# Kernel optimization log

Measured on AMD Instinct MI355X. Metric: run time of the kernel, lower is better.

## Reference

```python
import jax, jax.numpy as jnp
import numpy as np

MAX_REL = 30
N_HEADS = 8


def conv1d(x, w, b=None, groups=1):
    # x: [B, L, Cin], w: [Cout, Cin/groups, K]  (torch Conv1d layout), 'same' padding
    pad = w.shape[-1] // 2
    y = jax.lax.conv_general_dilated(
        x, w, window_strides=(1,), padding=[(pad, pad)],
        dimension_numbers=("NLC", "OIL", "NLC"), feature_group_count=groups)
    return y if b is None else y + b


def setup_inputs() -> dict:
    key = jax.random.key(0)
    ks = jax.random.split(key, 16)
    B, L, S = 8, 1024, 512          # L = 2 * S (required by Gamma.repeat(1,2,1))
    sd, vd, dm = 512, 64, 512       # spatial_dim == d_model (residual add)
    D = 3 * vd                      # rel-pos / K,V channel dim

    def n(k, shape, s):
        return (jax.random.normal(k, shape, jnp.float32) * s).astype(jnp.float32)

    return {
        "x_spatial": jax.random.normal(ks[0], (B, L, sd), jnp.float32),
        "x_velocity": jax.random.normal(ks[1], (B, S, vd), jnp.float32),
        "w_gamma": n(ks[2], (dm, vd, 1), 0.05)[:, :, 0],      # conv_gamma 1x1, no bias -> [dm, vd]
        "w3": n(ks[3], (vd, vd, 3), 0.07), "b3": jnp.zeros((vd,), jnp.float32),
        "w5": n(ks[4], (vd, vd, 5), 0.05), "b5": jnp.zeros((vd,), jnp.float32),
        "w7": n(ks[5], (vd, vd, 7), 0.04), "b7": jnp.zeros((vd,), jnp.float32),
        "rel_table": n(ks[6], (2 * MAX_REL + 1, D), 0.05),    # embedding [61, 192]
        "dw_w": n(ks[7], (D, 1, 3), 0.3), "dw_b": jnp.zeros((D,), jnp.float32),
        "wq": n(ks[8], (dm, sd), 0.03),
        "wk": n(ks[9], (dm, D), 0.05),
        "wv": n(ks[10], (dm, D), 0.05),
        "fc_w": n(ks[11], (dm, dm), 0.03), "fc_b": jnp.zeros((dm,), jnp.float32),
        "ln_g": jnp.ones((dm,), jnp.float32), "ln_b": jnp.zeros((dm,), jnp.float32),
    }


def rel_pos_enc(ms, rel_table, dw_w, dw_b):
    # Math-equivalent reduction of the torch O(B*S^2*D) op:
    # output[b,j] = mean_i where(i==j, dwconv_row_i(fused)[j], fused[b,i,j])
    #            = ms[b,j] + mean_i rel[i,j] + (diag_conv[b,j] - fused[b,j,j]) / S
    B, S, D = ms.shape
    pos = jnp.arange(S)
    idx = jnp.clip(pos[None, :] - pos[:, None], -MAX_REL, MAX_REL) + MAX_REL  # [S,S]
    mean_rel = rel_table[idx].mean(axis=0)                                    # [S,D]
    # fused[b,i,j] = ms[b,j] + rel_table[idx[i,j]]; diagonal uses idx = MAX_REL,
    # its +/-1 neighbors along j use MAX_REL -/+ ... -> rel[i,i-1]=MAX_REL-1, rel[i,i+1]=MAX_REL+1
    center = ms + rel_table[MAX_REL]                                          # fused[b,i,i]
    left = jnp.pad(ms[:, :-1] + rel_table[MAX_REL - 1], ((0, 0), (1, 0), (0, 0)))   # conv zero-pads at i=0
    right = jnp.pad(ms[:, 1:] + rel_table[MAX_REL + 1], ((0, 0), (0, 1), (0, 0)))   # conv zero-pads at i=S-1
    diag_conv = dw_w[:, 0, 0] * left + dw_w[:, 0, 1] * center + dw_w[:, 0, 2] * right + dw_b
    return ms + mean_rel[None] + (diag_conv - center) / S


def reference(x_spatial, x_velocity, w_gamma, w3, b3, w5, b5, w7, b7,
              rel_table, dw_w, dw_b, wq, wk, wv, fc_w, fc_b, ln_g, ln_b):
    B, S, vd = x_velocity.shape
    _, L, _ = x_spatial.shape
    dm = wq.shape[0]
    dk = dm // N_HEADS

    gamma = jax.nn.sigmoid(jnp.einsum("bsc,dc->bsd", x_velocity, w_gamma))   # [B,S,dm]

    ms = jnp.concatenate([conv1d(x_velocity, w3, b3),
                          conv1d(x_velocity, w5, b5),
                          conv1d(x_velocity, w7, b7)], axis=-1)              # [B,S,3vd]
    x_pe = rel_pos_enc(ms, rel_table, dw_w, dw_b)                            # [B,S,3vd]

    q = jnp.einsum("blc,dc->bld", x_spatial, wq).reshape(B, L, N_HEADS, dk).transpose(0, 2, 1, 3)
    k = jnp.einsum("bsc,dc->bsd", x_pe, wk).reshape(B, S, N_HEADS, dk).transpose(0, 2, 1, 3)
    v = jnp.einsum("bsc,dc->bsd", x_pe, wv).reshape(B, S, N_HEADS, dk).transpose(0, 2, 1, 3)

    scores = jnp.einsum("bhld,bhsd->bhls", q, k) / jnp.sqrt(jnp.float32(dk))
    attn = jax.nn.softmax(scores, axis=-1)                                   # dropout: eval mode (identity)
    out = jnp.einsum("bhls,bhsd->bhld", attn, v)                             # [B,H,L,dk]
    out = out.transpose(0, 2, 1, 3).reshape(B, L, dm)
    out = out @ fc_w.T + fc_b

    out = jnp.tile(gamma, (1, 2, 1)) * out                                   # L == 2*S
    res = x_spatial + out
    mu = res.mean(-1, keepdims=True)
    var = res.var(-1, keepdims=True)
    return (res - mu) / jnp.sqrt(var + 1e-5) * ln_g + ln_b
```

## Files before the change

kernel.cpp:

```cpp
#include <hip/hip_runtime.h>
#include <hip/hip_bf16.h>

constexpr int B  = 8;
constexpr int L  = 1024;
constexpr int S  = 512;
constexpr int VD = 64;
constexpr int DM = 512;
constexpr int D3 = 192;
constexpr int H  = 8;
constexpr int DK = 64;

typedef __attribute__((ext_vector_type(8))) short s8v;
typedef __attribute__((ext_vector_type(4))) float f4v;

__device__ inline unsigned short f2b(float f) {
    unsigned int u = __builtin_bit_cast(unsigned int, f);
    u += 0x7fffu + ((u >> 16) & 1u);
    return (unsigned short)(u >> 16);
}
__device__ inline float b2f(unsigned int lo16) {
    return __builtin_bit_cast(float, lo16 << 16);
}

__device__ __forceinline__ void gload16(const void* g, void* l) {
    __builtin_amdgcn_global_load_lds(
        (const __attribute__((address_space(1))) void*)g,
        (__attribute__((address_space(3))) void*)l, 16, 0, 0);
}

struct CastArgs {
    const float* src[7];
    unsigned short* dst[7];
    int n[7];
    float scale[7];
};

__global__ __launch_bounds__(256) void prep_cast_k(
    CastArgs a,
    const float* __restrict__ w3, const float* __restrict__ w5,
    const float* __restrict__ w7, const float* __restrict__ dw_w,
    const float* __restrict__ rel_table, const float* __restrict__ b3,
    const float* __restrict__ b5, const float* __restrict__ b7,
    const float* __restrict__ dw_b,
    unsigned short* __restrict__ WpeT, unsigned short* __restrict__ Cp)
{
    int t = threadIdx.x;
    int y = blockIdx.y;

    if (y < 7) {
        const float* s = a.src[y];
        unsigned short* d = a.dst[y];
        int n = a.n[y];
        float sc = a.scale[y];
        for (long i = (long)(blockIdx.x * 256 + t) * 4; i < n;
             i += (long)gridDim.x * 1024) {
            float4 f = *(const float4*)(s + i);
            ushort4 o;
            o.x = f2b(f.x * sc); o.y = f2b(f.y * sc);
            o.z = f2b(f.z * sc); o.w = f2b(f.w * sc);
            *(ushort4*)(d + i) = o;
        }
        return;
    }

    if (t >= 192) return;
    int o = t;
    float inv = 1.0f / S;

    if (blockIdx.x < 640) {
        int n = blockIdx.x;
        if (n >= 576) { WpeT[n * D3 + o] = 0; return; }
        int j = n >> 6, c = n & 63, delta = j - 4;
        const float* w; int KW, P, oo;
        if (o < 64)       { w = w3; KW = 3; P = 1; oo = o; }
        else if (o < 128) { w = w5; KW = 5; P = 2; oo = o - 64; }
        else              { w = w7; KW = 7; P = 3; oo = o - 128; }
        float mu0 = dw_w[o * 3 + 0] * inv;
        float mu1 = 1.f + (dw_w[o * 3 + 1] - 1.f) * inv;
        float mu2 = dw_w[o * 3 + 2] * inv;
        float acc = 0.f;
        int k;
        k = delta + 1 + P; if (k >= 0 && k < KW) acc += mu0 * w[(oo * 64 + c) * KW + k];
        k = delta + P;     if (k >= 0 && k < KW) acc += mu1 * w[(oo * 64 + c) * KW + k];
        k = delta - 1 + P; if (k >= 0 && k < KW) acc += mu2 * w[(oo * 64 + c) * KW + k];
        WpeT[n * D3 + o] = f2b(acc);
        return;
    }

    int j = blockIdx.x - 640;
    float acc = 0.f;
#pragma unroll
    for (int r = 1; r < 60; r++) {
        int i = j - (r - 30);
        if (i >= 0 && i < S) acc += rel_table[r * D3 + o];
    }
    float c60 = (float)max(0, j - 29);
    float c0  = (float)max(0, (S - 30) - j);
    acc += c60 * rel_table[60 * D3 + o] + c0 * rel_table[0 * D3 + o];
    float mean_rel = acc * inv;

    float bo  = (o < 64) ? b3[o] : (o < 128) ? b5[o - 64] : b7[o - 128];
    float dw0 = dw_w[o * 3], dw1 = dw_w[o * 3 + 1], dw2 = dw_w[o * 3 + 2];
    float r29 = rel_table[29 * D3 + o], r30 = rel_table[30 * D3 + o],
          r31 = rel_table[31 * D3 + o];
    float alpha = 1.f + (dw1 - 1.f) * inv, beta = dw0 * inv, gamma = dw2 * inv;

    float cp = mean_rel + bo * alpha + (dw1 * r30 + dw_b[o] - r30) * inv;
    if (j > 0)     cp += beta * bo + dw0 * r29 * inv;
    if (j < S - 1) cp += gamma * bo + dw2 * r31 * inv;
    Cp[j * D3 + o] = f2b(cp);
}

__global__ __launch_bounds__(256) void pre_gemm5_k(
    const unsigned short* __restrict__ wk_bf,
    const unsigned short* __restrict__ wv_bf,
    const unsigned short* __restrict__ WpeT,
    const unsigned short* __restrict__ Cp,
    const unsigned short* __restrict__ xv_bf,
    const unsigned short* __restrict__ wg_bf,
    unsigned short* __restrict__ WEff,
    unsigned short* __restrict__ Cb,
    unsigned short* __restrict__ gamma_bf)
{
    int z = blockIdx.z, mx = blockIdx.x, ny = blockIdx.y;
    const unsigned short *A, *Bm;
    unsigned short* C;
    int K, lda, ldb, ldc;
    if (z < 2) {
        if (mx >= 4) return;
        A = z ? wv_bf : wk_bf; Bm = WpeT; C = WEff + (long)z * DM * 640;
        K = D3; lda = D3; ldb = D3; ldc = 640;
    } else if (z < 4) {
        if (mx >= 4 || ny >= 4) return;
        A = Cp; Bm = (z == 2) ? wk_bf : wv_bf; C = Cb + (long)(z - 2) * S * DM;
        K = D3; lda = D3; ldb = D3; ldc = DM;
    } else {
        if (ny >= 4) return;
        A = xv_bf; Bm = wg_bf; C = gamma_bf;
        K = VD; lda = VD; ldb = VD; ldc = DM;
    }

    __shared__ __align__(16) unsigned short As[128 * 64];
    __shared__ __align__(16) unsigned short Bs[128 * 64];

    int t = threadIdx.x;
    int l = t & 63, w = t >> 6;
    int lx = l & 15, lh = l >> 4;
    int wr = w >> 1, wc = w & 1;
    int m0 = mx * 128, n0 = ny * 128;

    f4v acc[4][4] = {};

    for (int k0 = 0; k0 < K; k0 += 64) {
        __syncthreads();
#pragma unroll
        for (int p = 0; p < 4; p++) {
            int flat = p * 256 + t;
            int r = flat >> 3, c = flat & 7;
            int csw = (c ^ (r & 7)) * 8;
            gload16(A  + (long)(m0 + r) * lda + k0 + csw, As + flat * 8);
            gload16(Bm + (long)(n0 + r) * ldb + k0 + csw, Bs + flat * 8);
        }
        __syncthreads();
#pragma unroll
        for (int ks = 0; ks < 2; ks++) {
            s8v af[4], bf[4];
#pragma unroll
            for (int i = 0; i < 4; i++) {
                int ra = wr * 64 + i * 16 + lx;
                af[i] = *(const s8v*)(As + ra * 64 + (((ks * 4 + lh) ^ (ra & 7)) * 8));
                int rb = wc * 64 + i * 16 + lx;
                bf[i] = *(const s8v*)(Bs + rb * 64 + (((ks * 4 + lh) ^ (rb & 7)) * 8));
            }
#pragma unroll
            for (int i = 0; i < 4; i++)
#pragma unroll
                for (int j = 0; j < 4; j++)
                    acc[i][j] = __builtin_amdgcn_mfma_f32_16x16x32_bf16(
                        af[i], bf[j], acc[i][j], 0, 0, 0);
        }
    }

#pragma unroll
    for (int i = 0; i < 4; i++) {
#pragma unroll
        for (int r = 0; r < 4; r++) {
            int m = m0 + wr * 64 + i * 16 + lh * 4 + r;
#pragma unroll
            for (int j = 0; j < 4; j++) {
                int n = n0 + wc * 64 + j * 16 + lx;
                C[(long)m * ldc + n] = f2b(acc[i][j][r]);
            }
        }
    }
}

__global__ __launch_bounds__(256) void qconv_k(
    const unsigned short* __restrict__ xs_bf,
    const unsigned short* __restrict__ wq_bf,
    unsigned short* __restrict__ qbuf,
    const unsigned short* __restrict__ xvb,
    const unsigned short* __restrict__ Weff0,
    const unsigned short* __restrict__ bias0,
    unsigned short* __restrict__ Cout0,
    const unsigned short* __restrict__ zsrc)
{
    __shared__ __align__(16) unsigned short As[128 * 64];
    __shared__ __align__(16) unsigned short Bs[128 * 64];

    int zt = blockIdx.z;
    int t = threadIdx.x;
    int l = t & 63, w = t >> 6;
    int lx = l & 15, lh = l >> 4;
    int wr = w >> 1, wc = w & 1;

    f4v acc[4][4] = {};

    if (zt == 0) {
        int m0 = blockIdx.x * 128, n0 = blockIdx.y * 128;
        for (int k0 = 0; k0 < DM; k0 += 64) {
            __syncthreads();
#pragma unroll
            for (int p = 0; p < 4; p++) {
                int flat = p * 256 + t;
                int r = flat >> 3, c = flat & 7;
                int csw = (c ^ (r & 7)) * 8;
                gload16(xs_bf + (long)(m0 + r) * DM + k0 + csw, As + flat * 8);
                gload16(wq_bf + (long)(n0 + r) * DM + k0 + csw, Bs + flat * 8);
            }
            __syncthreads();
#pragma unroll
            for (int ks = 0; ks < 2; ks++) {
                s8v af[4], bf[4];
#pragma unroll
                for (int i = 0; i < 4; i++) {
                    int ra = wr * 64 + i * 16 + lx;
                    af[i] = *(const s8v*)(As + ra * 64 + (((ks * 4 + lh) ^ (ra & 7)) * 8));
                    int rb = wc * 64 + i * 16 + lx;
                    bf[i] = *(const s8v*)(Bs + rb * 64 + (((ks * 4 + lh) ^ (rb & 7)) * 8));
                }
#pragma unroll
                for (int i = 0; i < 4; i++)
#pragma unroll
                    for (int j = 0; j < 4; j++)
                        acc[i][j] = __builtin_amdgcn_mfma_f32_16x16x32_bf16(
                            af[i], bf[j], acc[i][j], 0, 0, 0);
            }
        }
#pragma unroll
        for (int i = 0; i < 4; i++) {
#pragma unroll
            for (int r = 0; r < 4; r++) {
                int m = m0 + wr * 64 + i * 16 + lh * 4 + r;
#pragma unroll
                for (int j = 0; j < 4; j++) {
                    int n = n0 + wc * 64 + j * 16 + lx;
                    qbuf[(long)m * DM + n] = f2b(acc[i][j][r]);
                }
            }
        }
        return;
    }

    if (blockIdx.x >= 32) return;
    int z = zt - 1;
    const unsigned short* Weff = Weff0 + (long)z * DM * 640;
    const unsigned short* bias2d = bias0 + (long)z * S * DM;
    unsigned short* Cout = Cout0 + (long)z * B * S * DM;

    int m0 = blockIdx.x * 128, n0 = blockIdx.y * 128;
    int b = m0 >> 9, s0 = m0 & 511;

    for (int j = 0; j < 9; j++) {
        __syncthreads();
#pragma unroll
        for (int p = 0; p < 4; p++) {
            int flat = p * 256 + t;
            int r = flat >> 3, c = flat & 7;
            int csw = (c ^ (r & 7)) * 8;
            int ss = s0 + r + j - 4;
            const unsigned short* asrc = (ss >= 0 && ss < S)
                ? xvb + ((long)b * S + ss) * VD + csw : zsrc;
            gload16(asrc, As + flat * 8);
            gload16(Weff + (long)(n0 + r) * 640 + j * 64 + csw, Bs + flat * 8);
        }
        __syncthreads();
#pragma unroll
        for (int ks = 0; ks < 2; ks++) {
            s8v af[4], bf[4];
#pragma unroll
            for (int i = 0; i < 4; i++) {
                int ra = wr * 64 + i * 16 + lx;
                af[i] = *(const s8v*)(As + ra * 64 + (((ks * 4 + lh) ^ (ra & 7)) * 8));
                int rb = wc * 64 + i * 16 + lx;
                bf[i] = *(const s8v*)(Bs + rb * 64 + (((ks * 4 + lh) ^ (rb & 7)) * 8));
            }
#pragma unroll
            for (int i = 0; i < 4; i++)
#pragma unroll
                for (int jj = 0; jj < 4; jj++)
                    acc[i][jj] = __builtin_amdgcn_mfma_f32_16x16x32_bf16(
                        af[i], bf[jj], acc[i][jj], 0, 0, 0);
        }
    }

#pragma unroll
    for (int i = 0; i < 4; i++) {
#pragma unroll
        for (int r = 0; r < 4; r++) {
            int m = m0 + wr * 64 + i * 16 + lh * 4 + r;
            int s = m & 511;
#pragma unroll
            for (int jj = 0; jj < 4; jj++) {
                int n = n0 + wc * 64 + jj * 16 + lx;
                Cout[(long)m * DM + n] =
                    f2b(acc[i][jj][r] + b2f(bias2d[(long)s * DM + n]));
            }
        }
    }
}

__global__ __launch_bounds__(256) void gemm_fc_k(
    const unsigned short* __restrict__ A, const unsigned short* __restrict__ Bm,
    unsigned short* __restrict__ Cout, const float* __restrict__ bias)
{
    __shared__ __align__(16) unsigned short As[128 * 64];
    __shared__ __align__(16) unsigned short Bs[128 * 64];

    int t = threadIdx.x;
    int l = t & 63, w = t >> 6;
    int lx = l & 15, lh = l >> 4;
    int wr = w >> 1, wc = w & 1;
    int m0 = blockIdx.x * 128, n0 = blockIdx.y * 128;

    f4v acc[4][4] = {};

    for (int k0 = 0; k0 < DM; k0 += 64) {
        __syncthreads();
#pragma unroll
        for (int p = 0; p < 4; p++) {
            int flat = p * 256 + t;
            int r = flat >> 3, c = flat & 7;
            int csw = (c ^ (r & 7)) * 8;
            gload16(A  + (long)(m0 + r) * DM + k0 + csw, As + flat * 8);
            gload16(Bm + (long)(n0 + r) * DM + k0 + csw, Bs + flat * 8);
        }
        __syncthreads();
#pragma unroll
        for (int ks = 0; ks < 2; ks++) {
            s8v af[4], bf[4];
#pragma unroll
            for (int i = 0; i < 4; i++) {
                int ra = wr * 64 + i * 16 + lx;
                af[i] = *(const s8v*)(As + ra * 64 + (((ks * 4 + lh) ^ (ra & 7)) * 8));
                int rb = wc * 64 + i * 16 + lx;
                bf[i] = *(const s8v*)(Bs + rb * 64 + (((ks * 4 + lh) ^ (rb & 7)) * 8));
            }
#pragma unroll
            for (int i = 0; i < 4; i++)
#pragma unroll
                for (int j = 0; j < 4; j++)
                    acc[i][j] = __builtin_amdgcn_mfma_f32_16x16x32_bf16(
                        af[i], bf[j], acc[i][j], 0, 0, 0);
        }
    }

#pragma unroll
    for (int i = 0; i < 4; i++) {
#pragma unroll
        for (int r = 0; r < 4; r++) {
            int m = m0 + wr * 64 + i * 16 + lh * 4 + r;
#pragma unroll
            for (int j = 0; j < 4; j++) {
                int n = n0 + wc * 64 + j * 16 + lx;
                Cout[(long)m * DM + n] = f2b(acc[i][j][r] + bias[n]);
            }
        }
    }
}

__global__ __launch_bounds__(256) void attn_mfma_k(
    const unsigned short* __restrict__ qb, const unsigned short* __restrict__ kb,
    const unsigned short* __restrict__ vb, unsigned short* __restrict__ ob)
{
    __shared__ __align__(16) unsigned short Qs[64 * 64];
    __shared__ __align__(16) unsigned short Ks[64 * 64];
    __shared__ __align__(16) unsigned short Vt[64 * 64];
    __shared__ __align__(16) unsigned short Ps[64 * 64];

    int lt = blockIdx.x, h = blockIdx.y, b = blockIdx.z;
    int t = threadIdx.x, l = t & 63, w = t >> 6, lx = l & 15, lh = l >> 4;

    const unsigned short* qg = qb + ((long)(b * L + lt * 64)) * DM + h * 64;
    const unsigned short* kg = kb + ((long)b * S) * DM + h * 64;
    const unsigned short* vg = vb + ((long)b * S) * DM + h * 64;

#pragma unroll
    for (int p = 0; p < 2; p++) {
        int flat = p * 256 + t;
        int r = flat >> 3, c = flat & 7;
        s8v v = *(const s8v*)(qg + (long)r * DM + c * 8);
        *(s8v*)(Qs + r * 64 + ((c ^ (r & 7)) * 8)) = v;
    }

    int kr0 = t >> 3, kc = t & 7;
    int vs = t & 63, vdq = t >> 6;
    s8v k0, k1, v0, v1;

    auto loadKV = [&](int st) {
        k0 = *(const s8v*)(kg + (long)(st * 64 + kr0) * DM + kc * 8);
        k1 = *(const s8v*)(kg + (long)(st * 64 + 32 + kr0) * DM + kc * 8);
        const unsigned short* vp = vg + (long)(st * 64 + vs) * DM + vdq * 16;
        v0 = *(const s8v*)(vp);
        v1 = *(const s8v*)(vp + 8);
    };
    auto writeKV = [&]() {
        *(s8v*)(Ks + kr0 * 64 + ((kc ^ (kr0 & 7)) * 8)) = k0;
        int r2 = 32 + kr0;
        *(s8v*)(Ks + r2 * 64 + ((kc ^ (r2 & 7)) * 8)) = k1;
#pragma unroll
        for (int e = 0; e < 8; e++) {
            int d1 = vdq * 16 + e;
            Vt[d1 * 64 + (((vs >> 3) ^ (d1 & 7)) * 8) + (vs & 7)] =
                (unsigned short)v0[e];
            int d2 = vdq * 16 + 8 + e;
            Vt[d2 * 64 + (((vs >> 3) ^ (d2 & 7)) * 8) + (vs & 7)] =
                (unsigned short)v1[e];
        }
    };

    loadKV(0);
    writeKV();
    __syncthreads();

    float lrow[4] = {0.f, 0.f, 0.f, 0.f};
    f4v oacc[4] = {};

    for (int st = 0; st < S / 64; st++) {
        if (st < S / 64 - 1) loadKV(st + 1);

        f4v pacc[4] = {};
        __builtin_amdgcn_s_setprio(1);
#pragma unroll
        for (int ks = 0; ks < 2; ks++) {
            int qr = w * 16 + lx;
            s8v a = *(const s8v*)(Qs + qr * 64 + (((ks * 4 + lh) ^ (qr & 7)) * 8));
#pragma unroll
            for (int jf = 0; jf < 4; jf++) {
                int kr = jf * 16 + lx;
                s8v bf = *(const s8v*)(Ks + kr * 64 + (((ks * 4 + lh) ^ (kr & 7)) * 8));
                pacc[jf] = __builtin_amdgcn_mfma_f32_16x16x32_bf16(a, bf, pacc[jf], 0, 0, 0);
            }
        }
        __builtin_amdgcn_s_setprio(0);

#pragma unroll
        for (int r = 0; r < 4; r++) {
            int prow = w * 16 + lh * 4 + r;
#pragma unroll
            for (int jf = 0; jf < 4; jf++) {
                float pe = __builtin_amdgcn_exp2f(pacc[jf][r]);
                lrow[r] += pe;
                int col = jf * 16 + lx;
                Ps[prow * 64 + (((col >> 3) ^ (prow & 7)) * 8) + (col & 7)] = f2b(pe);
            }
        }
        asm volatile("s_waitcnt lgkmcnt(0)" ::: "memory");

        __builtin_amdgcn_s_setprio(1);
#pragma unroll
        for (int ks2 = 0; ks2 < 2; ks2++) {
            int pr = w * 16 + lx;
            s8v pa = *(const s8v*)(Ps + pr * 64 + (((ks2 * 4 + lh) ^ (pr & 7)) * 8));
#pragma unroll
            for (int df = 0; df < 4; df++) {
                int vr = df * 16 + lx;
                s8v vf = *(const s8v*)(Vt + vr * 64 + (((ks2 * 4 + lh) ^ (vr & 7)) * 8));
                oacc[df] = __builtin_amdgcn_mfma_f32_16x16x32_bf16(pa, vf, oacc[df], 0, 0, 0);
            }
        }
        __builtin_amdgcn_s_setprio(0);
        __syncthreads();
        if (st < S / 64 - 1) {
            writeKV();
            __syncthreads();
        }
    }

    unsigned short* og = ob + ((long)(b * L + lt * 64 + w * 16)) * DM + h * 64;
#pragma unroll
    for (int r = 0; r < 4; r++) {
        float ls = lrow[r];
#pragma unroll
        for (int msk = 1; msk < 16; msk <<= 1) ls += __shfl_xor(ls, msk);
        float inv = 1.f / ls;
#pragma unroll
        for (int df = 0; df < 4; df++)
            og[(long)(lh * 4 + r) * DM + df * 16 + lx] = f2b(oacc[df][r] * inv);
    }
}

__global__ __launch_bounds__(256) void final_k(
    const float* __restrict__ xs, const unsigned short* __restrict__ fcb,
    const unsigned short* __restrict__ gb,
    const float* __restrict__ ln_g, const float* __restrict__ ln_b,
    float* __restrict__ out)
{
    int bl = blockIdx.x;
    int b = bl >> 10, lq = bl & 1023;
    int t = threadIdx.x;
    int d0 = t * 2;
    const unsigned short* g = gb + ((long)b * S + (lq & 511)) * DM;

    __shared__ float red[2][4];

    float2 xv = *(const float2*)(xs + (long)bl * DM + d0);
    unsigned int fp = *(const unsigned int*)(fcb + (long)bl * DM + d0);
    unsigned int gp = *(const unsigned int*)(g + d0);

    float fo0 = b2f(fp & 0xffffu), fo1 = b2f(fp >> 16);
    float ga0 = 1.f / (1.f + __expf(-b2f(gp & 0xffffu)));
    float ga1 = 1.f / (1.f + __expf(-b2f(gp >> 16)));
    float r0 = xv.x + ga0 * fo0;
    float r1 = xv.y + ga1 * fo1;

    float sum = r0 + r1, sumsq = r0 * r0 + r1 * r1;
#pragma unroll
    for (int msk = 1; msk < 64; msk <<= 1) {
        sum   += __shfl_xor(sum, msk);
        sumsq += __shfl_xor(sumsq, msk);
    }
    int wave = t >> 6;
    if ((t & 63) == 0) { red[0][wave] = sum; red[1][wave] = sumsq; }
    __syncthreads();
    float tot   = red[0][0] + red[0][1] + red[0][2] + red[0][3];
    float totsq = red[1][0] + red[1][1] + red[1][2] + red[1][3];

    float mu  = tot * (1.0f / DM);
    float var = totsq * (1.0f / DM) - mu * mu;
    float inv = rsqrtf(var + 1e-5f);

    float2 lg = *(const float2*)(ln_g + d0);
    float2 lb = *(const float2*)(ln_b + d0);
    float2 o;
    o.x = (r0 - mu) * inv * lg.x + lb.x;
    o.y = (r1 - mu) * inv * lg.y + lb.y;
    *(float2*)(out + (long)bl * DM + d0) = o;
}

extern "C" void kernel_launch(void* const* d_in, const int* in_sizes, int n_in,
                              void* d_out, int out_size, void* d_ws, size_t ws_size,
                              hipStream_t stream) {
    (void)in_sizes; (void)n_in; (void)out_size; (void)ws_size;

    const float* x_spatial  = (const float*)d_in[0];
    const float* x_velocity = (const float*)d_in[1];
    const float* w_gamma    = (const float*)d_in[2];
    const float* w3 = (const float*)d_in[3];
    const float* b3 = (const float*)d_in[4];
    const float* w5 = (const float*)d_in[5];
    const float* b5 = (const float*)d_in[6];
    const float* w7 = (const float*)d_in[7];
    const float* b7 = (const float*)d_in[8];
    const float* rel_table = (const float*)d_in[9];
    const float* dw_w = (const float*)d_in[10];
    const float* dw_b = (const float*)d_in[11];
    const float* wq   = (const float*)d_in[12];
    const float* wk   = (const float*)d_in[13];
    const float* wv   = (const float*)d_in[14];
    const float* fc_w = (const float*)d_in[15];
    const float* fc_b = (const float*)d_in[16];
    const float* ln_g = (const float*)d_in[17];
    const float* ln_b = (const float*)d_in[18];
    float* out = (float*)d_out;

    char* p = (char*)d_ws;
    auto alloc = [&](size_t bytes) {
        char* r = p;
        p += (bytes + 255) & ~(size_t)255;
        return r;
    };
    unsigned short* gamma_bf = (unsigned short*)alloc((size_t)B * S * DM * 2);
    unsigned short* fcb      = (unsigned short*)alloc((size_t)B * L * DM * 2);
    unsigned short* xs_bf   = (unsigned short*)alloc((size_t)B * L * DM * 2);
    unsigned short* xv_bf   = (unsigned short*)alloc((size_t)B * S * VD * 2);
    unsigned short* qbuf    = (unsigned short*)alloc((size_t)B * L * DM * 2);
    unsigned short* kbuf    = (unsigned short*)alloc((size_t)B * S * DM * 2);
    unsigned short* vbuf    = (unsigned short*)alloc((size_t)B * S * DM * 2);
    unsigned short* attn_bf = (unsigned short*)alloc((size_t)B * L * DM * 2);
    unsigned short* wq_bf   = (unsigned short*)alloc((size_t)DM * DM * 2);
    unsigned short* wk_bf   = (unsigned short*)alloc((size_t)DM * D3 * 2);
    unsigned short* wv_bf   = (unsigned short*)alloc((size_t)DM * D3 * 2);
    unsigned short* fcw_bf  = (unsigned short*)alloc((size_t)DM * DM * 2);
    unsigned short* wg_bf   = (unsigned short*)alloc((size_t)DM * VD * 2);
    unsigned short* WpeT    = (unsigned short*)alloc((size_t)640 * D3 * 2);
    unsigned short* Cp      = (unsigned short*)alloc((size_t)S * D3 * 2);
    unsigned short* WkEff   = (unsigned short*)alloc((size_t)DM * 640 * 2);
    unsigned short* WvEff   = (unsigned short*)alloc((size_t)DM * 640 * 2);
    unsigned short* Ckb     = (unsigned short*)alloc((size_t)S * DM * 2);
    unsigned short* Cvb     = (unsigned short*)alloc((size_t)S * DM * 2);
    (void)wv_bf; (void)WvEff; (void)Cvb;

    CastArgs ca;
    ca.src[0] = x_spatial;  ca.dst[0] = xs_bf;  ca.n[0] = B * L * DM; ca.scale[0] = 1.f;
    ca.src[1] = x_velocity; ca.dst[1] = xv_bf;  ca.n[1] = B * S * VD; ca.scale[1] = 1.f;
    ca.src[2] = wq;         ca.dst[2] = wq_bf;  ca.n[2] = DM * DM;    ca.scale[2] = 0.125f * 1.44269504089f;
    ca.src[3] = wk;         ca.dst[3] = wk_bf;  ca.n[3] = DM * D3;    ca.scale[3] = 1.f;
    ca.src[4] = wv;         ca.dst[4] = wv_bf;  ca.n[4] = DM * D3;    ca.scale[4] = 1.f;
    ca.src[5] = fc_w;       ca.dst[5] = fcw_bf; ca.n[5] = DM * DM;    ca.scale[5] = 1.f;
    ca.src[6] = w_gamma;    ca.dst[6] = wg_bf;  ca.n[6] = DM * VD;    ca.scale[6] = 1.f;
    prep_cast_k<<<dim3(1152, 8), 256, 0, stream>>>(
        ca, w3, w5, w7, dw_w, rel_table, b3, b5, b7, dw_b, WpeT, Cp);

    pre_gemm5_k<<<dim3(32, 5, 5), 256, 0, stream>>>(
        wk_bf, wv_bf, WpeT, Cp, xv_bf, wg_bf, WkEff, Ckb, gamma_bf);

    qconv_k<<<dim3(64, 4, 3), 256, 0, stream>>>(
        xs_bf, wq_bf, qbuf, xv_bf, WkEff, Ckb, kbuf,
        WkEff + 576 );

    attn_mfma_k<<<dim3(L / 64, H, B), 256, 0, stream>>>(qbuf, kbuf, vbuf, attn_bf);

    gemm_fc_k<<<dim3(64, 4), 256, 0, stream>>>(attn_bf, fcw_bf, fcb, fc_b);

    final_k<<<dim3(B * L), 256, 0, stream>>>(
        x_spatial, fcb, gamma_bf, ln_g, ln_b, out);
}
```

Before: 188.9 us.

## Fuse all stages into one persistent cooperative kernel with grid barriers

Replaces the chain of six kernel launches with a single cooperative persistent kernel that runs the cast, pre-GEMM, Q/conv GEMM, attention, FC and layernorm phases in sequence, separated by grid-wide syncs. Shared GEMM, conv, FC and attention bodies are factored into device functions reused by both paths. The aim is to remove launch gaps and per-kernel tail effects. In exchange the grid is capped at occupancy times CU count (at most 512 blocks), so large phases must loop over tiles, and every grid barrier adds its own sync cost. The old multi-kernel path is kept as a fallback if the cooperative launch fails.

```diff
diff --git a/kernel.cpp b/kernel.cpp
--- a/kernel.cpp
+++ b/kernel.cpp
@@ -1,5 +1,8 @@
 #include <hip/hip_runtime.h>
 #include <hip/hip_bf16.h>
+#include <hip/hip_cooperative_groups.h>
+
+namespace cg = cooperative_groups;
 
 constexpr int B  = 8;
 constexpr int L  = 1024;
@@ -8,7 +11,6 @@
 constexpr int DM = 512;
 constexpr int D3 = 192;
 constexpr int H  = 8;
-constexpr int DK = 64;
 
 typedef __attribute__((ext_vector_type(8))) short s8v;
 typedef __attribute__((ext_vector_type(4))) float f4v;
@@ -34,6 +36,309 @@
     int n[7];
     float scale[7];
 };
+
+struct Params {
+    const float *xs, *xv, *wg, *w3, *b3, *w5, *b5, *w7, *b7;
+    const float *rel, *dww, *dwb, *wq, *wk, *wv, *fcw, *fcbias, *lng, *lnb;
+    float* out;
+    unsigned short *xs_bf, *xv_bf, *wq_bf, *wk_bf, *wv_bf, *fcw_bf, *wg_bf;
+    unsigned short *WpeT, *Cp, *WkEff, *Ckb;
+    unsigned short *gamma_bf, *qbuf, *kvbuf, *attn_bf, *fcb;
+};
+
+
+__device__ __forceinline__ void gemm128_body(
+    const unsigned short* __restrict__ A, const unsigned short* __restrict__ Bm,
+    unsigned short* __restrict__ C, const float* __restrict__ bias,
+    int K, int lda, int ldb, int ldc, int m0, int n0,
+    unsigned short* As, unsigned short* Bs, int t)
+{
+    int l = t & 63, w = t >> 6;
+    int lx = l & 15, lh = l >> 4;
+    int wr = w >> 1, wc = w & 1;
+
+    f4v acc[4][4] = {};
+
+    for (int k0 = 0; k0 < K; k0 += 64) {
+        __syncthreads();
+#pragma unroll
+        for (int p = 0; p < 4; p++) {
+            int flat = p * 256 + t;
+            int r = flat >> 3, c = flat & 7;
+            int csw = (c ^ (r & 7)) * 8;
+            gload16(A  + (long)(m0 + r) * lda + k0 + csw, As + flat * 8);
+            gload16(Bm + (long)(n0 + r) * ldb + k0 + csw, Bs + flat * 8);
+        }
+        __syncthreads();
+#pragma unroll
+        for (int ks = 0; ks < 2; ks++) {
+            s8v af[4], bf[4];
+#pragma unroll
+            for (int i = 0; i < 4; i++) {
+                int ra = wr * 64 + i * 16 + lx;
+                af[i] = *(const s8v*)(As + ra * 64 + (((ks * 4 + lh) ^ (ra & 7)) * 8));
+                int rb = wc * 64 + i * 16 + lx;
+                bf[i] = *(const s8v*)(Bs + rb * 64 + (((ks * 4 + lh) ^ (rb & 7)) * 8));
+            }
+#pragma unroll
+            for (int i = 0; i < 4; i++)
+#pragma unroll
+                for (int j = 0; j < 4; j++)
+                    acc[i][j] = __builtin_amdgcn_mfma_f32_16x16x32_bf16(
+                        af[i], bf[j], acc[i][j], 0, 0, 0);
+        }
+    }
+
+#pragma unroll
+    for (int i = 0; i < 4; i++) {
+#pragma unroll
+        for (int r = 0; r < 4; r++) {
+            int m = m0 + wr * 64 + i * 16 + lh * 4 + r;
+#pragma unroll
+            for (int j = 0; j < 4; j++) {
+                int n = n0 + wc * 64 + j * 16 + lx;
+                float v = acc[i][j][r];
+                if (bias) v += bias[n];
+                C[(long)m * ldc + n] = f2b(v);
+            }
+        }
+    }
+}
+
+__device__ __forceinline__ void conv_body(
+    const unsigned short* __restrict__ xvb, const unsigned short* __restrict__ Weff,
+    const unsigned short* __restrict__ bias2d, unsigned short* __restrict__ Cout,
+    const unsigned short* __restrict__ zsrc, int m0, int n0,
+    unsigned short* As, unsigned short* Bs, int t)
+{
+    int l = t & 63, w = t >> 6;
+    int lx = l & 15, lh = l >> 4;
+    int wr = w >> 1, wc = w & 1;
+    int b = m0 >> 9, s0 = m0 & 511;
+
+    f4v acc[4][4] = {};
+
+    for (int j = 0; j < 9; j++) {
+        __syncthreads();
+#pragma unroll
+        for (int p = 0; p < 4; p++) {
+            int flat = p * 256 + t;
+            int r = flat >> 3, c = flat & 7;
+            int csw = (c ^ (r & 7)) * 8;
+            int ss = s0 + r + j - 4;
+            const unsigned short* asrc = (ss >= 0 && ss < S)
+                ? xvb + ((long)b * S + ss) * VD + csw : zsrc;
+            gload16(asrc, As + flat * 8);
+            gload16(Weff + (long)(n0 + r) * 640 + j * 64 + csw, Bs + flat * 8);
+        }
+        __syncthreads();
+#pragma unroll
+        for (int ks = 0; ks < 2; ks++) {
+            s8v af[4], bf[4];
+#pragma unroll
+            for (int i = 0; i < 4; i++) {
+                int ra = wr * 64 + i * 16 + lx;
+                af[i] = *(const s8v*)(As + ra * 64 + (((ks * 4 + lh) ^ (ra & 7)) * 8));
+                int rb = wc * 64 + i * 16 + lx;
+                bf[i] = *(const s8v*)(Bs + rb * 64 + (((ks * 4 + lh) ^ (rb & 7)) * 8));
+            }
+#pragma unroll
+            for (int i = 0; i < 4; i++)
+#pragma unroll
+                for (int jj = 0; jj < 4; jj++)
+                    acc[i][jj] = __builtin_amdgcn_mfma_f32_16x16x32_bf16(
+                        af[i], bf[jj], acc[i][jj], 0, 0, 0);
+        }
+    }
+
+#pragma unroll
+    for (int i = 0; i < 4; i++) {
+#pragma unroll
+        for (int r = 0; r < 4; r++) {
+            int m = m0 + wr * 64 + i * 16 + lh * 4 + r;
+            int s = m & 511;
+#pragma unroll
+            for (int jj = 0; jj < 4; jj++) {
+                int n = n0 + wc * 64 + jj * 16 + lx;
+                Cout[(long)m * DM + n] =
+                    f2b(acc[i][jj][r] + b2f(bias2d[(long)s * DM + n]));
+            }
+        }
+    }
+}
+
+__device__ __forceinline__ void fc64_body(
+    const unsigned short* __restrict__ A, const unsigned short* __restrict__ Bm,
+    unsigned short* __restrict__ C, const float* __restrict__ bias,
+    int m0, int n0, unsigned short* As, unsigned short* Bs, int t)
+{
+    int l = t & 63, w = t >> 6;
+    int lx = l & 15, lh = l >> 4;
+
+    f4v acc[2][4] = {};
+
+    for (int k0 = 0; k0 < DM; k0 += 64) {
+        __syncthreads();
+#pragma unroll
+        for (int p = 0; p < 4; p++) {
+            int flat = p * 256 + t;
+            int r = flat >> 3, c = flat & 7;
+            int csw = (c ^ (r & 7)) * 8;
+            gload16(A + (long)(m0 + r) * DM + k0 + csw, As + flat * 8);
+        }
+#pragma unroll
+        for (int p = 0; p < 2; p++) {
+            int flat = p * 256 + t;
+            int r = flat >> 3, c = flat & 7;
+            int csw = (c ^ (r & 7)) * 8;
+            gload16(Bm + (long)(n0 + r) * DM + k0 + csw, Bs + flat * 8);
+        }
+        __syncthreads();
+#pragma unroll
+        for (int ks = 0; ks < 2; ks++) {
+            s8v af[2], bf[4];
+#pragma unroll
+            for (int i = 0; i < 2; i++) {
+                int ra = w * 32 + i * 16 + lx;
+                af[i] = *(const s8v*)(As + ra * 64 + (((ks * 4 + lh) ^ (ra & 7)) * 8));
+            }
+#pragma unroll
+            for (int j = 0; j < 4; j++) {
+                int rb = j * 16 + lx;
+                bf[j] = *(const s8v*)(Bs + rb * 64 + (((ks * 4 + lh) ^ (rb & 7)) * 8));
+            }
+#pragma unroll
+            for (int i = 0; i < 2; i++)
+#pragma unroll
+                for (int j = 0; j < 4; j++)
+                    acc[i][j] = __builtin_amdgcn_mfma_f32_16x16x32_bf16(
+                        af[i], bf[j], acc[i][j], 0, 0, 0);
+        }
+    }
+
+#pragma unroll
+    for (int i = 0; i < 2; i++) {
+#pragma unroll
+        for (int r = 0; r < 4; r++) {
+            int m = m0 + w * 32 + i * 16 + lh * 4 + r;
+#pragma unroll
+            for (int j = 0; j < 4; j++) {
+                int n = n0 + j * 16 + lx;
+                C[(long)m * DM + n] = f2b(acc[i][j][r] + bias[n]);
+            }
+        }
+    }
+}
+
+__device__ __forceinline__ void attn_tile(
+    const unsigned short* __restrict__ qg, const unsigned short* __restrict__ kg,
+    const unsigned short* __restrict__ vg, unsigned short* __restrict__ obase,
+    unsigned short* Qs, unsigned short* Ks, unsigned short* Vt, unsigned short* Ps,
+    int t)
+{
+    int l = t & 63, w = t >> 6, lx = l & 15, lh = l >> 4;
+    int kr0 = t >> 3, kc = t & 7;
+    int vs = t & 63, vdq = t >> 6;
+
+#pragma unroll
+    for (int pp = 0; pp < 2; pp++) {
+        int flat = pp * 256 + t;
+        int r = flat >> 3, c = flat & 7;
+        s8v v = *(const s8v*)(qg + (long)r * DM + c * 8);
+        *(s8v*)(Qs + r * 64 + ((c ^ (r & 7)) * 8)) = v;
+    }
+
+    s8v k0, k1, v0, v1;
+    auto loadKV = [&](int st) {
+        k0 = *(const s8v*)(kg + (long)(st * 64 + kr0) * DM + kc * 8);
+        k1 = *(const s8v*)(kg + (long)(st * 64 + 32 + kr0) * DM + kc * 8);
+        const unsigned short* vp = vg + (long)(st * 64 + vs) * DM + vdq * 16;
+        v0 = *(const s8v*)(vp);
+        v1 = *(const s8v*)(vp + 8);
+    };
+    auto writeKV = [&]() {
+        *(s8v*)(Ks + kr0 * 64 + ((kc ^ (kr0 & 7)) * 8)) = k0;
+        int r2 = 32 + kr0;
+        *(s8v*)(Ks + r2 * 64 + ((kc ^ (r2 & 7)) * 8)) = k1;
+#pragma unroll
+        for (int e = 0; e < 8; e++) {
+            int d1 = vdq * 16 + e;
+            Vt[d1 * 64 + (((vs >> 3) ^ (d1 & 7)) * 8) + (vs & 7)] = (unsigned short)v0[e];
+            int d2 = vdq * 16 + 8 + e;
+            Vt[d2 * 64 + (((vs >> 3) ^ (d2 & 7)) * 8) + (vs & 7)] = (unsigned short)v1[e];
+        }
+    };
+
+    loadKV(0);
+    writeKV();
+    __syncthreads();
+
+    float lrow[4] = {0.f, 0.f, 0.f, 0.f};
+    f4v oacc[4] = {};
+
+    for (int st = 0; st < S / 64; st++) {
+        if (st < S / 64 - 1) loadKV(st + 1);
+
+        f4v pacc[4] = {};
+        __builtin_amdgcn_s_setprio(1);
+#pragma unroll
+        for (int ks = 0; ks < 2; ks++) {
+            int qr = w * 16 + lx;
+            s8v a = *(const s8v*)(Qs + qr * 64 + (((ks * 4 + lh) ^ (qr & 7)) * 8));
+#pragma unroll
+            for (int jf = 0; jf < 4; jf++) {
+                int kr = jf * 16 + lx;
+                s8v bf = *(const s8v*)(Ks + kr * 64 + (((ks * 4 + lh) ^ (kr & 7)) * 8));
+                pacc[jf] = __builtin_amdgcn_mfma_f32_16x16x32_bf16(a, bf, pacc[jf], 0, 0, 0);
+            }
+        }
+        __builtin_amdgcn_s_setprio(0);
+
+#pragma unroll
+        for (int r = 0; r < 4; r++) {
+            int prow = w * 16 + lh * 4 + r;
+#pragma unroll
+            for (int jf = 0; jf < 4; jf++) {
+                float pe = __builtin_amdgcn_exp2f(pacc[jf][r]);
+                lrow[r] += pe;
+                int col = jf * 16 + lx;
+                Ps[prow * 64 + (((col >> 3) ^ (prow & 7)) * 8) + (col & 7)] = f2b(pe);
+            }
+        }
+        asm volatile("s_waitcnt lgkmcnt(0)" ::: "memory");
+
+        __builtin_amdgcn_s_setprio(1);
+#pragma unroll
+        for (int ks2 = 0; ks2 < 2; ks2++) {
+            int pr = w * 16 + lx;
+            s8v pa = *(const s8v*)(Ps + pr * 64 + (((ks2 * 4 + lh) ^ (pr & 7)) * 8));
+#pragma unroll
+            for (int df = 0; df < 4; df++) {
+                int vr = df * 16 + lx;
+                s8v vf = *(const s8v*)(Vt + vr * 64 + (((ks2 * 4 + lh) ^ (vr & 7)) * 8));
+                oacc[df] = __builtin_amdgcn_mfma_f32_16x16x32_bf16(pa, vf, oacc[df], 0, 0, 0);
+            }
+        }
+        __builtin_amdgcn_s_setprio(0);
+        __syncthreads();
+        if (st < S / 64 - 1) {
+            writeKV();
+            __syncthreads();
+        }
+    }
+
+#pragma unroll
+    for (int r = 0; r < 4; r++) {
+        float ls = lrow[r];
+#pragma unroll
+        for (int msk = 1; msk < 16; msk <<= 1) ls += __shfl_xor(ls, msk);
+        float invl = 1.f / ls;
+#pragma unroll
+        for (int df = 0; df < 4; df++)
+            obase[(long)(w * 16 + lh * 4 + r) * DM + df * 16 + lx] = f2b(oacc[df][r] * invl);
+    }
+}
+
 
 __global__ __launch_bounds__(256) void prep_cast_k(
     CastArgs a,
@@ -142,57 +447,8 @@
 
     __shared__ __align__(16) unsigned short As[128 * 64];
     __shared__ __align__(16) unsigned short Bs[128 * 64];
-
-    int t = threadIdx.x;
-    int l = t & 63, w = t >> 6;
-    int lx = l & 15, lh = l >> 4;
-    int wr = w >> 1, wc = w & 1;
-    int m0 = mx * 128, n0 = ny * 128;
-
-    f4v acc[4][4] = {};
-
-    for (int k0 = 0; k0 < K; k0 += 64) {
-        __syncthreads();
-#pragma unroll
-        for (int p = 0; p < 4; p++) {
-            int flat = p * 256 + t;
-            int r = flat >> 3, c = flat & 7;
-            int csw = (c ^ (r & 7)) * 8;
-            gload16(A  + (long)(m0 + r) * lda + k0 + csw, As + flat * 8);
-            gload16(Bm + (long)(n0 + r) * ldb + k0 + csw, Bs + flat * 8);
-        }
-        __syncthreads();
-#pragma unroll
-        for (int ks = 0; ks < 2; ks++) {
-            s8v af[4], bf[4];
-#pragma unroll
-            for (int i = 0; i < 4; i++) {
-                int ra = wr * 64 + i * 16 + lx;
-                af[i] = *(const s8v*)(As + ra * 64 + (((ks * 4 + lh) ^ (ra & 7)) * 8));
-                int rb = wc * 64 + i * 16 + lx;
-                bf[i] = *(const s8v*)(Bs + rb * 64 + (((ks * 4 + lh) ^ (rb & 7)) * 8));
-            }
-#pragma unroll
-            for (int i = 0; i < 4; i++)
-#pragma unroll
-                for (int j = 0; j < 4; j++)
-                    acc[i][j] = __builtin_amdgcn_mfma_f32_16x16x32_bf16(
-                        af[i], bf[j], acc[i][j], 0, 0, 0);
-        }
-    }
-
-#pragma unroll
-    for (int i = 0; i < 4; i++) {
-#pragma unroll
-        for (int r = 0; r < 4; r++) {
-            int m = m0 + wr * 64 + i * 16 + lh * 4 + r;
-#pragma unroll
-            for (int j = 0; j < 4; j++) {
-                int n = n0 + wc * 64 + j * 16 + lx;
-                C[(long)m * ldc + n] = f2b(acc[i][j][r]);
-            }
-        }
-    }
+    gemm128_body(A, Bm, C, nullptr, K, lda, ldb, ldc,
+                 mx * 128, ny * 128, As, Bs, threadIdx.x);
 }
 
 __global__ __launch_bounds__(256) void qconv_k(
@@ -207,176 +463,18 @@
 {
     __shared__ __align__(16) unsigned short As[128 * 64];
     __shared__ __align__(16) unsigned short Bs[128 * 64];
-
-    int zt = blockIdx.z;
-    int t = threadIdx.x;
-    int l = t & 63, w = t >> 6;
-    int lx = l & 15, lh = l >> 4;
-    int wr = w >> 1, wc = w & 1;
-
-    f4v acc[4][4] = {};
+    int zt = blockIdx.z, t = threadIdx.x;
 
     if (zt == 0) {
-        int m0 = blockIdx.x * 128, n0 = blockIdx.y * 128;
-        for (int k0 = 0; k0 < DM; k0 += 64) {
-            __syncthreads();
-#pragma unroll
-            for (int p = 0; p < 4; p++) {
-                int flat = p * 256 + t;
-                int r = flat >> 3, c = flat & 7;
-                int csw = (c ^ (r & 7)) * 8;
-                gload16(xs_bf + (long)(m0 + r) * DM + k0 + csw, As + flat * 8);
-                gload16(wq_bf + (long)(n0 + r) * DM + k0 + csw, Bs + flat * 8);
-            }
-            __syncthreads();
-#pragma unroll
-            for (int ks = 0; ks < 2; ks++) {
-                s8v af[4], bf[4];
-#pragma unroll
-                for (int i = 0; i < 4; i++) {
-                    int ra = wr * 64 + i * 16 + lx;
-                    af[i] = *(const s8v*)(As + ra * 64 + (((ks * 4 + lh) ^ (ra & 7)) * 8));
-                    int rb = wc * 64 + i * 16 + lx;
-                    bf[i] = *(const s8v*)(Bs + rb * 64 + (((ks * 4 + lh) ^ (rb & 7)) * 8));
-                }
-#pragma unroll
-                for (int i = 0; i < 4; i++)
-#pragma unroll
-                    for (int j = 0; j < 4; j++)
-                        acc[i][j] = __builtin_amdgcn_mfma_f32_16x16x32_bf16(
-                            af[i], bf[j], acc[i][j], 0, 0, 0);
-            }
-        }
-#pragma unroll
-        for (int i = 0; i < 4; i++) {
-#pragma unroll
-            for (int r = 0; r < 4; r++) {
-                int m = m0 + wr * 64 + i * 16 + lh * 4 + r;
-#pragma unroll
-                for (int j = 0; j < 4; j++) {
-                    int n = n0 + wc * 64 + j * 16 + lx;
-                    qbuf[(long)m * DM + n] = f2b(acc[i][j][r]);
-                }
-            }
-        }
+        gemm128_body(xs_bf, wq_bf, qbuf, nullptr, DM, DM, DM, DM,
+                     blockIdx.x * 128, blockIdx.y * 128, As, Bs, t);
         return;
     }
-
     if (blockIdx.x >= 32) return;
     int z = zt - 1;
-    const unsigned short* Weff = Weff0 + (long)z * DM * 640;
-    const unsigned short* bias2d = bias0 + (long)z * S * DM;
-    unsigned short* Cout = Cout0 + (long)z * B * S * DM;
-
-    int m0 = blockIdx.x * 128, n0 = blockIdx.y * 128;
-    int b = m0 >> 9, s0 = m0 & 511;
-
-    for (int j = 0; j < 9; j++) {
-        __syncthreads();
-#pragma unroll
-        for (int p = 0; p < 4; p++) {
-            int flat = p * 256 + t;
-            int r = flat >> 3, c = flat & 7;
-            int csw = (c ^ (r & 7)) * 8;
-            int ss = s0 + r + j - 4;
-            const unsigned short* asrc = (ss >= 0 && ss < S)
-                ? xvb + ((long)b * S + ss) * VD + csw : zsrc;
-            gload16(asrc, As + flat * 8);
-            gload16(Weff + (long)(n0 + r) * 640 + j * 64 + csw, Bs + flat * 8);
-        }
-        __syncthreads();
-#pragma unroll
-        for (int ks = 0; ks < 2; ks++) {
-            s8v af[4], bf[4];
-#pragma unroll
-            for (int i = 0; i < 4; i++) {
-                int ra = wr * 64 + i * 16 + lx;
-                af[i] = *(const s8v*)(As + ra * 64 + (((ks * 4 + lh) ^ (ra & 7)) * 8));
-                int rb = wc * 64 + i * 16 + lx;
-                bf[i] = *(const s8v*)(Bs + rb * 64 + (((ks * 4 + lh) ^ (rb & 7)) * 8));
-            }
-#pragma unroll
-            for (int i = 0; i < 4; i++)
-#pragma unroll
-                for (int jj = 0; jj < 4; jj++)
-                    acc[i][jj] = __builtin_amdgcn_mfma_f32_16x16x32_bf16(
-                        af[i], bf[jj], acc[i][jj], 0, 0, 0);
-        }
-    }
-
-#pragma unroll
-    for (int i = 0; i < 4; i++) {
-#pragma unroll
-        for (int r = 0; r < 4; r++) {
-            int m = m0 + wr * 64 + i * 16 + lh * 4 + r;
-            int s = m & 511;
-#pragma unroll
-            for (int jj = 0; jj < 4; jj++) {
-                int n = n0 + wc * 64 + jj * 16 + lx;
-                Cout[(long)m * DM + n] =
-                    f2b(acc[i][jj][r] + b2f(bias2d[(long)s * DM + n]));
-            }
-        }
-    }
-}
-
-__global__ __launch_bounds__(256) void gemm_fc_k(
-    const unsigned short* __restrict__ A, const unsigned short* __restrict__ Bm,
-    unsigned short* __restrict__ Cout, const float* __restrict__ bias)
-{
-    __shared__ __align__(16) unsigned short As[128 * 64];
-    __shared__ __align__(16) unsigned short Bs[128 * 64];
-
-    int t = threadIdx.x;
-    int l = t & 63, w = t >> 6;
-    int lx = l & 15, lh = l >> 4;
-    int wr = w >> 1, wc = w & 1;
-    int m0 = blockIdx.x * 128, n0 = blockIdx.y * 128;
-
-    f4v acc[4][4] = {};
-
-    for (int k0 = 0; k0 < DM; k0 += 64) {
-        __syncthreads();
-#pragma unroll
-        for (int p = 0; p < 4; p++) {
-            int flat = p * 256 + t;
-            int r = flat >> 3, c = flat & 7;
-            int csw = (c ^ (r & 7)) * 8;
-            gload16(A  + (long)(m0 + r) * DM + k0 + csw, As + flat * 8);
-            gload16(Bm + (long)(n0 + r) * DM + k0 + csw, Bs + flat * 8);
-        }
-        __syncthreads();
-#pragma unroll
-        for (int ks = 0; ks < 2; ks++) {
-            s8v af[4], bf[4];
-#pragma unroll
-            for (int i = 0; i < 4; i++) {
-                int ra = wr * 64 + i * 16 + lx;
-                af[i] = *(const s8v*)(As + ra * 64 + (((ks * 4 + lh) ^ (ra & 7)) * 8));
-                int rb = wc * 64 + i * 16 + lx;
-                bf[i] = *(const s8v*)(Bs + rb * 64 + (((ks * 4 + lh) ^ (rb & 7)) * 8));
-            }
-#pragma unroll
-            for (int i = 0; i < 4; i++)
-#pragma unroll
-                for (int j = 0; j < 4; j++)
-                    acc[i][j] = __builtin_amdgcn_mfma_f32_16x16x32_bf16(
-                        af[i], bf[j], acc[i][j], 0, 0, 0);
-        }
-    }
-
-#pragma unroll
-    for (int i = 0; i < 4; i++) {
-#pragma unroll
-        for (int r = 0; r < 4; r++) {
-            int m = m0 + wr * 64 + i * 16 + lh * 4 + r;
-#pragma unroll
-            for (int j = 0; j < 4; j++) {
-                int n = n0 + wc * 64 + j * 16 + lx;
-                Cout[(long)m * DM + n] = f2b(acc[i][j][r] + bias[n]);
-            }
-        }
-    }
+    conv_body(xvb, Weff0 + (long)z * DM * 640, bias0 + (long)z * S * DM,
+              Cout0 + (long)z * B * S * DM, zsrc,
+              blockIdx.x * 128, blockIdx.y * 128, As, Bs, t);
 }
 
 __global__ __launch_bounds__(256) void attn_mfma_k(
@@ -389,115 +487,21 @@
     __shared__ __align__(16) unsigned short Ps[64 * 64];
 
     int lt = blockIdx.x, h = blockIdx.y, b = blockIdx.z;
-    int t = threadIdx.x, l = t & 63, w = t >> 6, lx = l & 15, lh = l >> 4;
-
-    const unsigned short* qg = qb + ((long)(b * L + lt * 64)) * DM + h * 64;
-    const unsigned short* kg = kb + ((long)b * S) * DM + h * 64;
-    const unsigned short* vg = vb + ((long)b * S) * DM + h * 64;
-
-#pragma unroll
-    for (int p = 0; p < 2; p++) {
-        int flat = p * 256 + t;
-        int r = flat >> 3, c = flat & 7;
-        s8v v = *(const s8v*)(qg + (long)r * DM + c * 8);
-        *(s8v*)(Qs + r * 64 + ((c ^ (r & 7)) * 8)) = v;
-    }
-
-    int kr0 = t >> 3, kc = t & 7;
-    int vs = t & 63, vdq = t >> 6;
-    s8v k0, k1, v0, v1;
-
-    auto loadKV = [&](int st) {
-        k0 = *(const s8v*)(kg + (long)(st * 64 + kr0) * DM + kc * 8);
-        k1 = *(const s8v*)(kg + (long)(st * 64 + 32 + kr0) * DM + kc * 8);
-        const unsigned short* vp = vg + (long)(st * 64 + vs) * DM + vdq * 16;
-        v0 = *(const s8v*)(vp);
-        v1 = *(const s8v*)(vp + 8);
-    };
-    auto writeKV = [&]() {
-        *(s8v*)(Ks + kr0 * 64 + ((kc ^ (kr0 & 7)) * 8)) = k0;
-        int r2 = 32 + kr0;
-        *(s8v*)(Ks + r2 * 64 + ((kc ^ (r2 & 7)) * 8)) = k1;
-#pragma unroll
-        for (int e = 0; e < 8; e++) {
-            int d1 = vdq * 16 + e;
-            Vt[d1 * 64 + (((vs >> 3) ^ (d1 & 7)) * 8) + (vs & 7)] =
-                (unsigned short)v0[e];
-            int d2 = vdq * 16 + 8 + e;
-            Vt[d2 * 64 + (((vs >> 3) ^ (d2 & 7)) * 8) + (vs & 7)] =
-                (unsigned short)v1[e];
-        }
-    };
-
-    loadKV(0);
-    writeKV();
-    __syncthreads();
-
-    float lrow[4] = {0.f, 0.f, 0.f, 0.f};
-    f4v oacc[4] = {};
-
-    for (int st = 0; st < S / 64; st++) {
-        if (st < S / 64 - 1) loadKV(st + 1);
-
-        f4v pacc[4] = {};
-        __builtin_amdgcn_s_setprio(1);
-#pragma unroll
-        for (int ks = 0; ks < 2; ks++) {
-            int qr = w * 16 + lx;
-            s8v a = *(const s8v*)(Qs + qr * 64 + (((ks * 4 + lh) ^ (qr & 7)) * 8));
-#pragma unroll
-            for (int jf = 0; jf < 4; jf++) {
-                int kr = jf * 16 + lx;
-                s8v bf = *(const s8v*)(Ks + kr * 64 + (((ks * 4 + lh) ^ (kr & 7)) * 8));
-                pacc[jf] = __builtin_amdgcn_mfma_f32_16x16x32_bf16(a, bf, pacc[jf], 0, 0, 0);
-            }
-        }
-        __builtin_amdgcn_s_setprio(0);
-
-#pragma unroll
-        for (int r = 0; r < 4; r++) {
-            int prow = w * 16 + lh * 4 + r;
-#pragma unroll
-            for (int jf = 0; jf < 4; jf++) {
-                float pe = __builtin_amdgcn_exp2f(pacc[jf][r]);
-                lrow[r] += pe;
-                int col = jf * 16 + lx;
-                Ps[prow * 64 + (((col >> 3) ^ (prow & 7)) * 8) + (col & 7)] = f2b(pe);
-            }
-        }
-        asm volatile("s_waitcnt lgkmcnt(0)" ::: "memory");
-
-        __builtin_amdgcn_s_setprio(1);
-#pragma unroll
-        for (int ks2 = 0; ks2 < 2; ks2++) {
-            int pr = w * 16 + lx;
-            s8v pa = *(const s8v*)(Ps + pr * 64 + (((ks2 * 4 + lh) ^ (pr & 7)) * 8));
-#pragma unroll
-            for (int df = 0; df < 4; df++) {
-                int vr = df * 16 + lx;
-                s8v vf = *(const s8v*)(Vt + vr * 64 + (((ks2 * 4 + lh) ^ (vr & 7)) * 8));
-                oacc[df] = __builtin_amdgcn_mfma_f32_16x16x32_bf16(pa, vf, oacc[df], 0, 0, 0);
-            }
-        }
-        __builtin_amdgcn_s_setprio(0);
-        __syncthreads();
-        if (st < S / 64 - 1) {
-            writeKV();
-            __syncthreads();
-        }
-    }
-
-    unsigned short* og = ob + ((long)(b * L + lt * 64 + w * 16)) * DM + h * 64;
-#pragma unroll
-    for (int r = 0; r < 4; r++) {
-        float ls = lrow[r];
-#pragma unroll
-        for (int msk = 1; msk < 16; msk <<= 1) ls += __shfl_xor(ls, msk);
-        float inv = 1.f / ls;
-#pragma unroll
-        for (int df = 0; df < 4; df++)
-            og[(long)(lh * 4 + r) * DM + df * 16 + lx] = f2b(oacc[df][r] * inv);
-    }
+    attn_tile(qb + ((long)(b * L + lt * 64)) * DM + h * 64,
+              kb + ((long)b * S) * DM + h * 64,
+              vb + ((long)b * S) * DM + h * 64,
+              ob + ((long)(b * L + lt * 64)) * DM + h * 64,
+              Qs, Ks, Vt, Ps, threadIdx.x);
+}
+
+__global__ __launch_bounds__(256) void gemm_fc_k(
+    const unsigned short* __restrict__ A, const unsigned short* __restrict__ Bm,
+    unsigned short* __restrict__ Cout, const float* __restrict__ bias)
+{
+    __shared__ __align__(16) unsigned short As[128 * 64];
+    __shared__ __align__(16) unsigned short Bs[128 * 64];
+    gemm128_body(A, Bm, Cout, bias, DM, DM, DM, DM,
+                 blockIdx.x * 128, blockIdx.y * 128, As, Bs, threadIdx.x);
 }
 
 __global__ __launch_bounds__(256) void final_k(
@@ -514,15 +518,15 @@
 
     __shared__ float red[2][4];
 
-    float2 xv = *(const float2*)(xs + (long)bl * DM + d0);
+    float2 xv2 = *(const float2*)(xs + (long)bl * DM + d0);
     unsigned int fp = *(const unsigned int*)(fcb + (long)bl * DM + d0);
     unsigned int gp = *(const unsigned int*)(g + d0);
 
     float fo0 = b2f(fp & 0xffffu), fo1 = b2f(fp >> 16);
     float ga0 = 1.f / (1.f + __expf(-b2f(gp & 0xffffu)));
     float ga1 = 1.f / (1.f + __expf(-b2f(gp >> 16)));
-    float r0 = xv.x + ga0 * fo0;
-    float r1 = xv.y + ga1 * fo1;
+    float r0 = xv2.x + ga0 * fo0;
+    float r1 = xv2.y + ga1 * fo1;
 
     float sum = r0 + r1, sumsq = r0 * r0 + r1 * r1;
 #pragma unroll
@@ -548,81 +552,292 @@
     *(float2*)(out + (long)bl * DM + d0) = o;
 }
 
+__global__ __launch_bounds__(256, 2) void fused_k(Params p) {
+    __shared__ __align__(16) unsigned short lds[16384];
+    unsigned short* As = lds;
+    unsigned short* Bs = lds + 8192;
+
+    int t   = threadIdx.x;
+    int blk = blockIdx.x;
+    int nbl = gridDim.x;
+    cg::grid_group grid = cg::this_grid();
+
+    {
+        const float* srcs[7] = {p.xs, p.xv, p.wq, p.wk, p.wv, p.fcw, p.wg};
+        unsigned short* dsts[7] = {p.xs_bf, p.xv_bf, p.wq_bf, p.wk_bf,
+                                   p.wv_bf, p.fcw_bf, p.wg_bf};
+        const int   ns[7] = {B * L * DM, B * S * VD, DM * DM, DM * D3,
+                             DM * D3, DM * DM, DM * VD};
+        const float scs[7] = {1.f, 1.f, 0.125f * 1.44269504089f, 1.f, 1.f, 1.f, 1.f};
+#pragma unroll
+        for (int id = 0; id < 7; id++) {
+            const float* s = srcs[id];
+            unsigned short* d = dsts[id];
+            float sc = scs[id];
+            for (long i = (long)(blk * 256 + t) * 4; i < ns[id];
+                 i += (long)nbl * 1024) {
+                float4 f = *(const float4*)(s + i);
+                ushort4 o;
+                o.x = f2b(f.x * sc); o.y = f2b(f.y * sc);
+                o.z = f2b(f.z * sc); o.w = f2b(f.w * sc);
+                *(ushort4*)(d + i) = o;
+            }
+        }
+
+        float inv = 1.0f / S;
+        if (t < 192) {
+            int o = t;
+            for (int row = blk; row < 1152; row += nbl) {
+                if (row < 640) {
+                    int n = row;
+                    if (n >= 576) { p.WpeT[n * D3 + o] = 0; continue; }
+                    int j = n >> 6, c = n & 63, delta = j - 4;
+                    const float* w; int KW, P, oo;
+                    if (o < 64)       { w = p.w3; KW = 3; P = 1; oo = o; }
+                    else if (o < 128) { w = p.w5; KW = 5; P = 2; oo = o - 64; }
+                    else              { w = p.w7; KW = 7; P = 3; oo = o - 128; }
+                    float mu0 = p.dww[o * 3 + 0] * inv;
+                    float mu1 = 1.f + (p.dww[o * 3 + 1] - 1.f) * inv;
+                    float mu2 = p.dww[o * 3 + 2] * inv;
+                    float acc = 0.f;
+                    int k;
+                    k = delta + 1 + P; if (k >= 0 && k < KW) acc += mu0 * w[(oo * 64 + c) * KW + k];
+                    k = delta + P;     if (k >= 0 && k < KW) acc += mu1 * w[(oo * 64 + c) * KW + k];
+                    k = delta - 1 + P; if (k >= 0 && k < KW) acc += mu2 * w[(oo * 64 + c) * KW + k];
+                    p.WpeT[n * D3 + o] = f2b(acc);
+                } else {
+                    int j = row - 640;
+                    float acc = 0.f;
+#pragma unroll
+                    for (int r = 1; r < 60; r++) {
+                        int i = j - (r - 30);
+                        if (i >= 0 && i < S) acc += p.rel[r * D3 + o];
+                    }
+                    float c60 = (float)max(0, j - 29);
+                    float c0  = (float)max(0, (S - 30) - j);
+                    acc += c60 * p.rel[60 * D3 + o] + c0 * p.rel[0 * D3 + o];
+                    float mean_rel = acc * inv;
+
+                    float bo  = (o < 64) ? p.b3[o] : (o < 128) ? p.b5[o - 64] : p.b7[o - 128];
+                    float dw0 = p.dww[o * 3], dw1 = p.dww[o * 3 + 1], dw2 = p.dww[o * 3 + 2];
+                    float r29 = p.rel[29 * D3 + o], r30 = p.rel[30 * D3 + o],
+                          r31 = p.rel[31 * D3 + o];
+                    float alpha = 1.f + (dw1 - 1.f) * inv, beta = dw0 * inv, gamma = dw2 * inv;
+
+                    float cp = mean_rel + bo * alpha + (dw1 * r30 + p.dwb[o] - r30) * inv;
+                    if (j > 0)     cp += beta * bo + dw0 * r29 * inv;
+                    if (j < S - 1) cp += gamma * bo + dw2 * r31 * inv;
+                    p.Cp[j * D3 + o] = f2b(cp);
+                }
+            }
+        }
+    }
+    grid.sync();
+
+    for (int vb = blk; vb < 200; vb += nbl) {
+        if (vb < 20) {
+            gemm128_body(p.wk_bf, p.WpeT, p.WkEff, nullptr,
+                         D3, D3, D3, 640, (vb / 5) * 128, (vb % 5) * 128, As, Bs, t);
+        } else if (vb < 40) {
+            int i = vb - 20;
+            gemm128_body(p.wv_bf, p.WpeT, p.WkEff + (long)DM * 640, nullptr,
+                         D3, D3, D3, 640, (i / 5) * 128, (i % 5) * 128, As, Bs, t);
+        } else if (vb < 56) {
+            int i = vb - 40;
+            gemm128_body(p.Cp, p.wk_bf, p.Ckb, nullptr,
+                         D3, D3, D3, DM, (i / 4) * 128, (i % 4) * 128, As, Bs, t);
+        } else if (vb < 72) {
+            int i = vb - 56;
+            gemm128_body(p.Cp, p.wv_bf, p.Ckb + (long)S * DM, nullptr,
+                         D3, D3, D3, DM, (i / 4) * 128, (i % 4) * 128, As, Bs, t);
+        } else {
+            int i = vb - 72;
+            gemm128_body(p.xv_bf, p.wg_bf, p.gamma_bf, nullptr,
+                         VD, VD, VD, DM, (i >> 2) * 128, (i & 3) * 128, As, Bs, t);
+        }
+        __syncthreads();
+    }
+    grid.sync();
+
+    {
+        const unsigned short* zsrc = p.WkEff + 576;
+        for (int vb = blk; vb < 512; vb += nbl) {
+            if (vb < 256) {
+                gemm128_body(p.xs_bf, p.wq_bf, p.qbuf, nullptr,
+                             DM, DM, DM, DM, (vb >> 2) * 128, (vb & 3) * 128, As, Bs, t);
+            } else {
+                int i = vb - 256;
+                int z = i >> 7, rem = i & 127;
+                conv_body(p.xv_bf, p.WkEff + (long)z * DM * 640,
+                          p.Ckb + (long)z * S * DM, p.kvbuf + (long)z * B * S * DM,
+                          zsrc, (rem >> 2) * 128, (rem & 3) * 128, As, Bs, t);
+            }
+            __syncthreads();
+        }
+    }
+    grid.sync();
+
+    {
+        unsigned short* Qs = lds;
+        unsigned short* Ks = lds + 4096;
+        unsigned short* Vt = lds + 8192;
+        unsigned short* Ps = lds + 12288;
+
+        for (int ti = blk; ti < 1024; ti += nbl) {
+            int lt = ti & 15, h = (ti >> 4) & 7, b = ti >> 7;
+            attn_tile(p.qbuf + ((long)(b * L + lt * 64)) * DM + h * 64,
+                      p.kvbuf + ((long)b * S) * DM + h * 64,
+                      p.kvbuf + (long)B * S * DM + ((long)b * S) * DM + h * 64,
+                      p.attn_bf + ((long)(b * L + lt * 64)) * DM + h * 64,
+                      Qs, Ks, Vt, Ps, t);
+            __syncthreads();
+        }
+    }
+    grid.sync();
+
+    for (int vb = blk; vb < 512; vb += nbl) {
+        fc64_body(p.attn_bf, p.fcw_bf, p.fcb, p.fcbias,
+                  (vb >> 3) * 128, (vb & 7) * 64, As, Bs, t);
+        __syncthreads();
+    }
+    grid.sync();
+
+    {
+        float* red = (float*)lds;
+        int d0 = t * 2;
+        for (int bl = blk; bl < B * L; bl += nbl) {
+            int b = bl >> 10, lq = bl & 1023;
+            const unsigned short* g = p.gamma_bf + ((long)b * S + (lq & 511)) * DM;
+
+            float2 xv2 = *(const float2*)(p.xs + (long)bl * DM + d0);
+            unsigned int fp = *(const unsigned int*)(p.fcb + (long)bl * DM + d0);
+            unsigned int gp = *(const unsigned int*)(g + d0);
+
+            float fo0 = b2f(fp & 0xffffu), fo1 = b2f(fp >> 16);
+            float ga0 = 1.f / (1.f + __expf(-b2f(gp & 0xffffu)));
+            float ga1 = 1.f / (1.f + __expf(-b2f(gp >> 16)));
+            float r0 = xv2.x + ga0 * fo0;
+            float r1 = xv2.y + ga1 * fo1;
+
+            float sum = r0 + r1, sumsq = r0 * r0 + r1 * r1;
+#pragma unroll
+            for (int msk = 1; msk < 64; msk <<= 1) {
+                sum   += __shfl_xor(sum, msk);
+                sumsq += __shfl_xor(sumsq, msk);
+            }
+            int wave = t >> 6;
+            if ((t & 63) == 0) { red[wave] = sum; red[4 + wave] = sumsq; }
+            __syncthreads();
+            float tot   = red[0] + red[1] + red[2] + red[3];
+            float totsq = red[4] + red[5] + red[6] + red[7];
+            __syncthreads();
+
+            float mu  = tot * (1.0f / DM);
+            float var = totsq * (1.0f / DM) - mu * mu;
+            float inv = rsqrtf(var + 1e-5f);
+
+            float2 lg = *(const float2*)(p.lng + d0);
+            float2 lb = *(const float2*)(p.lnb + d0);
+            float2 o;
+            o.x = (r0 - mu) * inv * lg.x + lb.x;
+            o.y = (r1 - mu) * inv * lg.y + lb.y;
+            *(float2*)(p.out + (long)bl * DM + d0) = o;
+        }
+    }
+}
+
 extern "C" void kernel_launch(void* const* d_in, const int* in_sizes, int n_in,
                               void* d_out, int out_size, void* d_ws, size_t ws_size,
                               hipStream_t stream) {
     (void)in_sizes; (void)n_in; (void)out_size; (void)ws_size;
 
-    const float* x_spatial  = (const float*)d_in[0];
-    const float* x_velocity = (const float*)d_in[1];
-    const float* w_gamma    = (const float*)d_in[2];
-    const float* w3 = (const float*)d_in[3];
-    const float* b3 = (const float*)d_in[4];
-    const float* w5 = (const float*)d_in[5];
-    const float* b5 = (const float*)d_in[6];
-    const float* w7 = (const float*)d_in[7];
-    const float* b7 = (const float*)d_in[8];
-    const float* rel_table = (const float*)d_in[9];
-    const float* dw_w = (const float*)d_in[10];
-    const float* dw_b = (const float*)d_in[11];
-    const float* wq   = (const float*)d_in[12];
-    const float* wk   = (const float*)d_in[13];
-    const float* wv   = (const float*)d_in[14];
-    const float* fc_w = (const float*)d_in[15];
-    const float* fc_b = (const float*)d_in[16];
-    const float* ln_g = (const float*)d_in[17];
-    const float* ln_b = (const float*)d_in[18];
-    float* out = (float*)d_out;
-
-    char* p = (char*)d_ws;
+    char* pw = (char*)d_ws;
     auto alloc = [&](size_t bytes) {
-        char* r = p;
-        p += (bytes + 255) & ~(size_t)255;
+        char* r = pw;
+        pw += (bytes + 255) & ~(size_t)255;
         return r;
     };
-    unsigned short* gamma_bf = (unsigned short*)alloc((size_t)B * S * DM * 2);
-    unsigned short* fcb      = (unsigned short*)alloc((size_t)B * L * DM * 2);
-    unsigned short* xs_bf   = (unsigned short*)alloc((size_t)B * L * DM * 2);
-    unsigned short* xv_bf   = (unsigned short*)alloc((size_t)B * S * VD * 2);
-    unsigned short* qbuf    = (unsigned short*)alloc((size_t)B * L * DM * 2);
-    unsigned short* kbuf    = (unsigned short*)alloc((size_t)B * S * DM * 2);
-    unsigned short* vbuf    = (unsigned short*)alloc((size_t)B * S * DM * 2);
-    unsigned short* attn_bf = (unsigned short*)alloc((size_t)B * L * DM * 2);
-    unsigned short* wq_bf   = (unsigned short*)alloc((size_t)DM * DM * 2);
-    unsigned short* wk_bf   = (unsigned short*)alloc((size_t)DM * D3 * 2);
-    unsigned short* wv_bf   = (unsigned short*)alloc((size_t)DM * D3 * 2);
-    unsigned short* fcw_bf  = (unsigned short*)alloc((size_t)DM * DM * 2);
-    unsigned short* wg_bf   = (unsigned short*)alloc((size_t)DM * VD * 2);
-    unsigned short* WpeT    = (unsigned short*)alloc((size_t)640 * D3 * 2);
-    unsigned short* Cp      = (unsigned short*)alloc((size_t)S * D3 * 2);
-    unsigned short* WkEff   = (unsigned short*)alloc((size_t)DM * 640 * 2);
-    unsigned short* WvEff   = (unsigned short*)alloc((size_t)DM * 640 * 2);
-    unsigned short* Ckb     = (unsigned short*)alloc((size_t)S * DM * 2);
-    unsigned short* Cvb     = (unsigned short*)alloc((size_t)S * DM * 2);
-    (void)wv_bf; (void)WvEff; (void)Cvb;
+
+    Params p;
+    p.xs  = (const float*)d_in[0];
+    p.xv  = (const float*)d_in[1];
+    p.wg  = (const float*)d_in[2];
+    p.w3  = (const float*)d_in[3];
+    p.b3  = (const float*)d_in[4];
+    p.w5  = (const float*)d_in[5];
+    p.b5  = (const float*)d_in[6];
+    p.w7  = (const float*)d_in[7];
+    p.b7  = (const float*)d_in[8];
+    p.rel = (const float*)d_in[9];
+    p.dww = (const float*)d_in[10];
+    p.dwb = (const float*)d_in[11];
+    p.wq  = (const float*)d_in[12];
+    p.wk  = (const float*)d_in[13];
+    p.wv  = (const float*)d_in[14];
+    p.fcw = (const float*)d_in[15];
+    p.fcbias = (const float*)d_in[16];
+    p.lng = (const float*)d_in[17];
+    p.lnb = (const float*)d_in[18];
+    p.out = (float*)d_out;
+
+    p.gamma_bf = (unsigned short*)alloc((size_t)B * S * DM * 2);
+    p.fcb      = (unsigned short*)alloc((size_t)B * L * DM * 2);
+    p.xs_bf    = (unsigned short*)alloc((size_t)B * L * DM * 2);
+    p.xv_bf    = (unsigned short*)alloc((size_t)B * S * VD * 2);
+    p.qbuf     = (unsigned short*)alloc((size_t)B * L * DM * 2);
+    p.kvbuf    = (unsigned short*)alloc((size_t)2 * B * S * DM * 2);
+    p.attn_bf  = (unsigned short*)alloc((size_t)B * L * DM * 2);
+    p.wq_bf    = (unsigned short*)alloc((size_t)DM * DM * 2);
+    p.wk_bf    = (unsigned short*)alloc((size_t)DM * D3 * 2);
+    p.wv_bf    = (unsigned short*)alloc((size_t)DM * D3 * 2);
+    p.fcw_bf   = (unsigned short*)alloc((size_t)DM * DM * 2);
+    p.wg_bf    = (unsigned short*)alloc((size_t)DM * VD * 2);
+    p.WpeT     = (unsigned short*)alloc((size_t)640 * D3 * 2);
+    p.Cp       = (unsigned short*)alloc((size_t)S * D3 * 2);
+    p.WkEff    = (unsigned short*)alloc((size_t)2 * DM * 640 * 2);
+    p.Ckb      = (unsigned short*)alloc((size_t)2 * S * DM * 2);
+
+    int dev = 0, coop = 0, ncu = 0, maxb = 0;
+    bool ok = (hipGetDevice(&dev) == hipSuccess);
+    if (ok) ok = (hipDeviceGetAttribute(&coop, hipDeviceAttributeCooperativeLaunch, dev)
+                  == hipSuccess) && coop;
+    if (ok) ok = (hipDeviceGetAttribute(&ncu, hipDeviceAttributeMultiprocessorCount, dev)
+                  == hipSuccess) && ncu > 0;
+    if (ok) ok = (hipOccupancyMaxActiveBlocksPerMultiprocessor(&maxb, fused_k, 256, 0)
+                  == hipSuccess) && maxb >= 1;
+    if (ok) {
+        int g = maxb * ncu;
+        if (g > 512) g = 512;
+        void* args[] = {&p};
+        if (hipLaunchCooperativeKernel((const void*)fused_k, dim3(g), dim3(256),
+                                       args, 0, stream) == hipSuccess)
+            return;
+        (void)hipGetLastError();
+    }
 
     CastArgs ca;
-    ca.src[0] = x_spatial;  ca.dst[0] = xs_bf;  ca.n[0] = B * L * DM; ca.scale[0] = 1.f;
-    ca.src[1] = x_velocity; ca.dst[1] = xv_bf;  ca.n[1] = B * S * VD; ca.scale[1] = 1.f;
-    ca.src[2] = wq;         ca.dst[2] = wq_bf;  ca.n[2] = DM * DM;    ca.scale[2] = 0.125f * 1.44269504089f;
-    ca.src[3] = wk;         ca.dst[3] = wk_bf;  ca.n[3] = DM * D3;    ca.scale[3] = 1.f;
-    ca.src[4] = wv;         ca.dst[4] = wv_bf;  ca.n[4] = DM * D3;    ca.scale[4] = 1.f;
-    ca.src[5] = fc_w;       ca.dst[5] = fcw_bf; ca.n[5] = DM * DM;    ca.scale[5] = 1.f;
-    ca.src[6] = w_gamma;    ca.dst[6] = wg_bf;  ca.n[6] = DM * VD;    ca.scale[6] = 1.f;
+    ca.src[0] = p.xs;  ca.dst[0] = p.xs_bf;  ca.n[0] = B * L * DM; ca.scale[0] = 1.f;
+    ca.src[1] = p.xv;  ca.dst[1] = p.xv_bf;  ca.n[1] = B * S * VD; ca.scale[1] = 1.f;
+    ca.src[2] = p.wq;  ca.dst[2] = p.wq_bf;  ca.n[2] = DM * DM;    ca.scale[2] = 0.125f * 1.44269504089f;
+    ca.src[3] = p.wk;  ca.dst[3] = p.wk_bf;  ca.n[3] = DM * D3;    ca.scale[3] = 1.f;
+    ca.src[4] = p.wv;  ca.dst[4] = p.wv_bf;  ca.n[4] = DM * D3;    ca.scale[4] = 1.f;
+    ca.src[5] = p.fcw; ca.dst[5] = p.fcw_bf; ca.n[5] = DM * DM;    ca.scale[5] = 1.f;
+    ca.src[6] = p.wg;  ca.dst[6] = p.wg_bf;  ca.n[6] = DM * VD;    ca.scale[6] = 1.f;
+
     prep_cast_k<<<dim3(1152, 8), 256, 0, stream>>>(
-        ca, w3, w5, w7, dw_w, rel_table, b3, b5, b7, dw_b, WpeT, Cp);
+        ca, p.w3, p.w5, p.w7, p.dww, p.rel, p.b3, p.b5, p.b7, p.dwb, p.WpeT, p.Cp);
 
     pre_gemm5_k<<<dim3(32, 5, 5), 256, 0, stream>>>(
-        wk_bf, wv_bf, WpeT, Cp, xv_bf, wg_bf, WkEff, Ckb, gamma_bf);
+        p.wk_bf, p.wv_bf, p.WpeT, p.Cp, p.xv_bf, p.wg_bf, p.WkEff, p.Ckb, p.gamma_bf);
 
     qconv_k<<<dim3(64, 4, 3), 256, 0, stream>>>(
-        xs_bf, wq_bf, qbuf, xv_bf, WkEff, Ckb, kbuf,
-        WkEff + 576 );
-
-    attn_mfma_k<<<dim3(L / 64, H, B), 256, 0, stream>>>(qbuf, kbuf, vbuf, attn_bf);
-
-    gemm_fc_k<<<dim3(64, 4), 256, 0, stream>>>(attn_bf, fcw_bf, fcb, fc_b);
+        p.xs_bf, p.wq_bf, p.qbuf, p.xv_bf, p.WkEff, p.Ckb, p.kvbuf, p.WkEff + 576);
+
+    attn_mfma_k<<<dim3(L / 64, H, B), 256, 0, stream>>>(
+        p.qbuf, p.kvbuf, p.kvbuf + (long)B * S * DM, p.attn_bf);
+
+    gemm_fc_k<<<dim3(64, 4), 256, 0, stream>>>(p.attn_bf, p.fcw_bf, p.fcb, p.fcbias);
 
     final_k<<<dim3(B * L), 256, 0, stream>>>(
-        x_spatial, fcb, gamma_bf, ln_g, ln_b, out);
-}
+        p.xs, p.fcb, p.gamma_bf, p.lng, p.lnb, p.out);
+}
```

Result: slower. 414.4 us (+119.3%).
